# Kernel tuning notes

Measured on AMD Instinct MI355X. Metric: run time of the kernel, lower is better.

## Reference

```python
import jax, jax.numpy as jnp
import numpy as np

# opt hyperparameters (from init_kwargs)
L = 16        # number of multipath taps
M = 64        # number of subcarriers (FFT size for H_t)
N_PILOT = 2   # pilot symbols
V = 100.0     # velocity used for Doppler shift


def setup_inputs() -> dict:
    key = jax.random.key(0)
    k1, k2, k3, k4 = jax.random.split(key, 4)
    N, P, S, MK = 1024, 8, 14, 80
    SMK = S * MK  # 1120
    return {
        "input_real": jax.random.normal(k1, (N, P, SMK), dtype=jnp.float32),
        "input_imag": jax.random.normal(k2, (N, P, SMK), dtype=jnp.float32),
        "cof_real": jax.random.normal(k3, (N, P, L), dtype=jnp.float32),
        "cof_imag": jax.random.normal(k4, (N, P, L), dtype=jnp.float32),
        "Ns": 12,
    }


def reference(input_real, input_imag, cof_real, cof_imag, Ns):
    N, P, SMK = input_real.shape
    S = Ns + N_PILOT
    x = (input_real + 1j * input_imag).astype(jnp.complex64)   # (N,P,SMK)
    cof = (cof_real + 1j * cof_imag).astype(jnp.complex64)      # (N,P,L)

    # H_t: FFT of zero-padded channel taps along delay dim
    cof_zp = jnp.concatenate([cof, jnp.zeros((N, P, M - L), dtype=cof.dtype)], axis=-1)
    H_t = jnp.fft.fft(cof_zp, axis=-1)                          # (N,P,M)

    # Doppler phase shifts: shift[l,s] = exp(i * 2*pi*cos(angle_l)*fd * t_s)
    t = jnp.linspace(0.0, (S - 1) * (0.0005 / 14.0), S)         # (S,)
    carrier_freq = 3.0e9
    max_doppler = V / 3.0e8 * carrier_freq
    angles = jnp.linspace(0.0, 2.0 * np.pi, L)                  # (L,)
    phases = jnp.outer(2.0 * np.pi * jnp.cos(angles) * max_doppler, t)  # (L,S)
    shift = jnp.exp(1j * phases).astype(jnp.complex64)          # (L,S)

    # out[n,p,s,k] = sum_l x[n,p,s,k] * cof[n,p,l] * shift[l,s]
    # The sum over L factors out of the MK dim -> fused weight, avoiding the
    # (N,P,L,S,MK) broadcast intermediate the original materializes.
    weight = jnp.einsum('npl,ls->nps', cof, shift)              # (N,P,S)
    out = x.reshape(N, P, S, -1) * weight[..., None]            # (N,P,S,MK)
    output = out.reshape(N, P, SMK)
    return output, H_t
```

## Files before the change

### kernel.cpp

```cpp
#include <hip/hip_runtime.h>
#include <math.h>

#define L_TAPS 16
#define M_FFT  64
#define SMAX   256
#define SMK_MAX 2048

__global__ __launch_bounds__(256) void channel_kernel(
    const float* __restrict__ xr, const float* __restrict__ xi,
    const float* __restrict__ cr, const float* __restrict__ ci,
    const int*   __restrict__ ns_ptr,
    float* __restrict__ out,
    int NP, int SMK, int interleaved)
{
    __shared__ float  s_cr[L_TAPS], s_ci[L_TAPS];
    __shared__ float2 s_w[SMAX];
    __shared__ unsigned short s_smap[SMK_MAX];

    const int np  = blockIdx.x;
    const int tid = threadIdx.x;
    const int S   = ns_ptr[0] + 2;
    const int MK  = SMK / S;

    if (tid < L_TAPS) {
        s_cr[tid] = cr[(size_t)np * L_TAPS + tid];
        s_ci[tid] = ci[(size_t)np * L_TAPS + tid];
    }
    __syncthreads();

    for (int i = tid; i < SMK; i += 256) {
        s_smap[i] = (unsigned short)(i / MK);
    }

    if (tid < S && tid < SMAX) {
        const float two_pi = 6.2831853071795864f;
        const float dt     = 0.0005f / 14.0f;
        const float fd     = 100.0f / 3.0e8f * 3.0e9f;
        const float t      = tid * dt;
        float wr_ = 0.f, wi_ = 0.f;
        #pragma unroll
        for (int l = 0; l < L_TAPS; ++l) {
            float angle = l * (two_pi / 15.0f);
            float phase = two_pi * __cosf(angle) * fd * t;
            float sp, cp;
            __sincosf(phase, &sp, &cp);
            wr_ += s_cr[l] * cp - s_ci[l] * sp;
            wi_ += s_cr[l] * sp + s_ci[l] * cp;
        }
        s_w[tid] = make_float2(wr_, wi_);
    }

    if (tid >= 64 && tid < 64 + M_FFT) {
        const int m = tid - 64;
        float hr = 0.f, hi = 0.f;
        #pragma unroll
        for (int l = 0; l < L_TAPS; ++l) {
            int ml = (m * l) & (M_FFT - 1);
            float theta = -(float)ml * (6.2831853071795864f / 64.0f);
            float sp, cp;
            __sincosf(theta, &sp, &cp);
            hr += s_cr[l] * cp - s_ci[l] * sp;
            hi += s_cr[l] * sp + s_ci[l] * cp;
        }
        const size_t hbase = (size_t)NP * SMK;
        if (interleaved) {
            ((float2*)out)[hbase + (size_t)np * M_FFT + m] = make_float2(hr, hi);
        } else {
            out[hbase + (size_t)np * M_FFT + m] = hr;
        }
    }
    __syncthreads();

    const size_t base = (size_t)np * SMK;
    if ((MK & 3) == 0 && (SMK & 3) == 0) {
        const float4* xr4 = (const float4*)(xr + base);
        const float4* xi4 = (const float4*)(xi + base);
        const int nvec = SMK >> 2;
        for (int i = tid; i < nvec; i += 256) {
            float4 a = xr4[i];
            float4 b = xi4[i];
            float2 w = s_w[s_smap[i << 2]];
            float4 re;
            re.x = a.x * w.x - b.x * w.y;
            re.y = a.y * w.x - b.y * w.y;
            re.z = a.z * w.x - b.z * w.y;
            re.w = a.w * w.x - b.w * w.y;
            if (interleaved) {
                float2* o = ((float2*)out) + base;
                o[(i << 2) + 0] = make_float2(re.x, a.x * w.y + b.x * w.x);
                o[(i << 2) + 1] = make_float2(re.y, a.y * w.y + b.y * w.x);
                o[(i << 2) + 2] = make_float2(re.z, a.z * w.y + b.z * w.x);
                o[(i << 2) + 3] = make_float2(re.w, a.w * w.y + b.w * w.x);
            } else {
                ((float4*)(out + base))[i] = re;
            }
        }
    } else {
        for (int i = tid; i < SMK; i += 256) {
            float xre = xr[base + i];
            float xim = xi[base + i];
            float2 w  = s_w[s_smap[i]];
            if (interleaved) {
                ((float2*)out)[base + i] = make_float2(xre * w.x - xim * w.y,
                                                       xre * w.y + xim * w.x);
            } else {
                out[base + i] = xre * w.x - xim * w.y;
            }
        }
    }
}

extern "C" void kernel_launch(void* const* d_in, const int* in_sizes, int n_in,
                              void* d_out, int out_size, void* d_ws, size_t ws_size,
                              hipStream_t stream) {
    const float* xr = (const float*)d_in[0];
    const float* xi = (const float*)d_in[1];
    const float* cr = (const float*)d_in[2];
    const float* ci = (const float*)d_in[3];
    const int*   ns = (const int*)  d_in[4];

    const int NP  = in_sizes[2] / L_TAPS;
    const int SMK = in_sizes[0] / NP;

    const int elems = NP * SMK + NP * M_FFT;
    const int interleaved = (out_size == 2 * elems) ? 1 : 0;

    channel_kernel<<<NP, 256, 0, stream>>>(xr, xi, cr, ci, ns,
                                           (float*)d_out, NP, SMK, interleaved);
}
```

Baseline: 23.87 us.

## Split into weight/H_t kernel and grid-stride streaming multiply kernel

The single per-row kernel becomes two kernels. The first computes the per-row Doppler weights into workspace and writes H_t from a shared twiddle table, handling four rows per block. The second is a flat grid-stride elementwise multiply over all rows with float4 loads, so work is no longer tied to one block per row. This removes the per-block smap division table and the redundant sincos work, at the cost of an extra launch and a round trip of the weights through global memory.

```diff
diff --git a/kernel.cpp b/kernel.cpp
--- a/kernel.cpp
+++ b/kernel.cpp
@@ -3,110 +3,110 @@
 
 #define L_TAPS 16
 #define M_FFT  64
-#define SMAX   256
-#define SMK_MAX 2048
 
-__global__ __launch_bounds__(256) void channel_kernel(
-    const float* __restrict__ xr, const float* __restrict__ xi,
+__global__ __launch_bounds__(256) void weight_ht_kernel(
     const float* __restrict__ cr, const float* __restrict__ ci,
     const int*   __restrict__ ns_ptr,
-    float* __restrict__ out,
+    float2* __restrict__ ws,
+    float*  __restrict__ out,
     int NP, int SMK, int interleaved)
 {
-    __shared__ float  s_cr[L_TAPS], s_ci[L_TAPS];
-    __shared__ float2 s_w[SMAX];
-    __shared__ unsigned short s_smap[SMK_MAX];
+    __shared__ float2 s_tw[M_FFT];
+    __shared__ float  s_dop[L_TAPS];
+    __shared__ float2 s_cof[4][L_TAPS];
 
-    const int np  = blockIdx.x;
-    const int tid = threadIdx.x;
-    const int S   = ns_ptr[0] + 2;
-    const int MK  = SMK / S;
+    const int tid  = threadIdx.x;
+    const int S    = ns_ptr[0] + 2;
+    const int row0 = blockIdx.x * 4;
+    const int row  = tid >> 6;
+    const int lane = tid & 63;
+    const int np   = row0 + row;
 
-    if (tid < L_TAPS) {
-        s_cr[tid] = cr[(size_t)np * L_TAPS + tid];
-        s_ci[tid] = ci[(size_t)np * L_TAPS + tid];
+    const float two_pi = 6.2831853071795864f;
+
+    if (tid < 64) {
+        float sp, cp;
+        __sincosf(-(float)tid * (two_pi / 64.0f), &sp, &cp);
+        s_tw[tid] = make_float2(cp, sp);
+    } else if (tid < 64 + L_TAPS) {
+        int l = tid - 64;
+        s_dop[l] = two_pi * __cosf(l * (two_pi / 15.0f)) * (100.0f / 3.0e8f * 3.0e9f);
+    } else if (tid >= 128 && tid < 192) {
+        int r = (tid - 128) >> 4;
+        int l = tid & 15;
+        int npp = row0 + r;
+        if (npp < NP)
+            s_cof[r][l] = make_float2(cr[(size_t)npp * L_TAPS + l],
+                                      ci[(size_t)npp * L_TAPS + l]);
     }
     __syncthreads();
 
-    for (int i = tid; i < SMK; i += 256) {
-        s_smap[i] = (unsigned short)(i / MK);
-    }
+    if (np >= NP) return;
 
-    if (tid < S && tid < SMAX) {
-        const float two_pi = 6.2831853071795864f;
-        const float dt     = 0.0005f / 14.0f;
-        const float fd     = 100.0f / 3.0e8f * 3.0e9f;
-        const float t      = tid * dt;
-        float wr_ = 0.f, wi_ = 0.f;
-        #pragma unroll
-        for (int l = 0; l < L_TAPS; ++l) {
-            float angle = l * (two_pi / 15.0f);
-            float phase = two_pi * __cosf(angle) * fd * t;
-            float sp, cp;
-            __sincosf(phase, &sp, &cp);
-            wr_ += s_cr[l] * cp - s_ci[l] * sp;
-            wi_ += s_cr[l] * sp + s_ci[l] * cp;
-        }
-        s_w[tid] = make_float2(wr_, wi_);
-    }
-
-    if (tid >= 64 && tid < 64 + M_FFT) {
-        const int m = tid - 64;
+    {
+        const int m = lane;
         float hr = 0.f, hi = 0.f;
         #pragma unroll
         for (int l = 0; l < L_TAPS; ++l) {
-            int ml = (m * l) & (M_FFT - 1);
-            float theta = -(float)ml * (6.2831853071795864f / 64.0f);
-            float sp, cp;
-            __sincosf(theta, &sp, &cp);
-            hr += s_cr[l] * cp - s_ci[l] * sp;
-            hi += s_cr[l] * sp + s_ci[l] * cp;
+            float2 c = s_cof[row][l];
+            float2 t = s_tw[(m * l) & (M_FFT - 1)];
+            hr += c.x * t.x - c.y * t.y;
+            hi += c.x * t.y + c.y * t.x;
         }
         const size_t hbase = (size_t)NP * SMK;
-        if (interleaved) {
+        if (interleaved)
             ((float2*)out)[hbase + (size_t)np * M_FFT + m] = make_float2(hr, hi);
-        } else {
+        else
             out[hbase + (size_t)np * M_FFT + m] = hr;
+    }
+
+    if (lane < S) {
+        const float t = lane * (0.0005f / 14.0f);
+        float wr = 0.f, wi = 0.f;
+        #pragma unroll
+        for (int l = 0; l < L_TAPS; ++l) {
+            float sp, cp;
+            __sincosf(s_dop[l] * t, &sp, &cp);
+            float2 c = s_cof[row][l];
+            wr += c.x * cp - c.y * sp;
+            wi += c.x * sp + c.y * cp;
         }
+        ws[np * S + lane] = make_float2(wr, wi);
     }
-    __syncthreads();
+}
 
-    const size_t base = (size_t)np * SMK;
-    if ((MK & 3) == 0 && (SMK & 3) == 0) {
-        const float4* xr4 = (const float4*)(xr + base);
-        const float4* xi4 = (const float4*)(xi + base);
-        const int nvec = SMK >> 2;
-        for (int i = tid; i < nvec; i += 256) {
-            float4 a = xr4[i];
-            float4 b = xi4[i];
-            float2 w = s_w[s_smap[i << 2]];
-            float4 re;
-            re.x = a.x * w.x - b.x * w.y;
-            re.y = a.y * w.x - b.y * w.y;
-            re.z = a.z * w.x - b.z * w.y;
-            re.w = a.w * w.x - b.w * w.y;
-            if (interleaved) {
-                float2* o = ((float2*)out) + base;
-                o[(i << 2) + 0] = make_float2(re.x, a.x * w.y + b.x * w.x);
-                o[(i << 2) + 1] = make_float2(re.y, a.y * w.y + b.y * w.x);
-                o[(i << 2) + 2] = make_float2(re.z, a.z * w.y + b.z * w.x);
-                o[(i << 2) + 3] = make_float2(re.w, a.w * w.y + b.w * w.x);
-            } else {
-                ((float4*)(out + base))[i] = re;
-            }
-        }
-    } else {
-        for (int i = tid; i < SMK; i += 256) {
-            float xre = xr[base + i];
-            float xim = xi[base + i];
-            float2 w  = s_w[s_smap[i]];
-            if (interleaved) {
-                ((float2*)out)[base + i] = make_float2(xre * w.x - xim * w.y,
-                                                       xre * w.y + xim * w.x);
-            } else {
-                out[base + i] = xre * w.x - xim * w.y;
-            }
-        }
+__global__ __launch_bounds__(256) void stream_kernel_v4(
+    const float4* __restrict__ xr4, const float4* __restrict__ xi4,
+    const float2* __restrict__ ws,
+    float4* __restrict__ out4, int nvec, int mkq)
+{
+    const int stride = gridDim.x * blockDim.x;
+    for (int v = blockIdx.x * blockDim.x + threadIdx.x; v < nvec; v += stride) {
+        float4 a = xr4[v];
+        float4 b = xi4[v];
+        float2 w = ws[v / mkq];
+        float4 r;
+        r.x = a.x * w.x - b.x * w.y;
+        r.y = a.y * w.x - b.y * w.y;
+        r.z = a.z * w.x - b.z * w.y;
+        r.w = a.w * w.x - b.w * w.y;
+        out4[v] = r;
+    }
+}
+
+__global__ __launch_bounds__(256) void stream_kernel_scalar(
+    const float* __restrict__ xr, const float* __restrict__ xi,
+    const float2* __restrict__ ws,
+    float* __restrict__ out, int n, int MK, int interleaved)
+{
+    const int stride = gridDim.x * blockDim.x;
+    for (int i = blockIdx.x * blockDim.x + threadIdx.x; i < n; i += stride) {
+        float2 w = ws[i / MK];
+        float  a = xr[i], b = xi[i];
+        if (interleaved)
+            ((float2*)out)[i] = make_float2(a * w.x - b * w.y, a * w.y + b * w.x);
+        else
+            out[i] = a * w.x - b * w.y;
     }
 }
 
@@ -125,6 +125,55 @@
     const int elems = NP * SMK + NP * M_FFT;
     const int interleaved = (out_size == 2 * elems) ? 1 : 0;
 
-    channel_kernel<<<NP, 256, 0, stream>>>(xr, xi, cr, ci, ns,
-                                           (float*)d_out, NP, SMK, interleaved);
+    float2* ws  = (float2*)d_ws;
+    float*  out = (float*)d_out;
+
+    weight_ht_kernel<<<(NP + 3) / 4, 256, 0, stream>>>(cr, ci, ns, ws, out,
+                                                       NP, SMK, interleaved);
+
+    (void)ws_size;
+    extern __global__ void stream_dispatch(const float4*, const float4*,
+                                           const float2*, const int*,
+                                           float*, int, int, int);
+    stream_dispatch<<<2048, 256, 0, stream>>>((const float4*)xr, (const float4*)xi,
+                                              ws, ns, out, NP, SMK, interleaved);
 }
+
+__global__ __launch_bounds__(256) void stream_dispatch(
+    const float4* __restrict__ xr4, const float4* __restrict__ xi4,
+    const float2* __restrict__ ws, const int* __restrict__ ns_ptr,
+    float* __restrict__ out, int NP, int SMK, int interleaved)
+{
+    const int S  = ns_ptr[0] + 2;
+    const int MK = SMK / S;
+    const int n  = NP * SMK;
+    const int stride = gridDim.x * blockDim.x;
+
+    if (!interleaved && (MK & 3) == 0) {
+        const int nvec = n >> 2;
+        const int mkq  = MK >> 2;
+        float4* out4 = (float4*)out;
+        for (int v = blockIdx.x * blockDim.x + threadIdx.x; v < nvec; v += stride) {
+            float4 a = xr4[v];
+            float4 b = xi4[v];
+            float2 w = ws[v / mkq];
+            float4 r;
+            r.x = a.x * w.x - b.x * w.y;
+            r.y = a.y * w.x - b.y * w.y;
+            r.z = a.z * w.x - b.z * w.y;
+            r.w = a.w * w.x - b.w * w.y;
+            out4[v] = r;
+        }
+    } else {
+        const float* xr = (const float*)xr4;
+        const float* xi = (const float*)xi4;
+        for (int i = blockIdx.x * blockDim.x + threadIdx.x; i < n; i += stride) {
+            float2 w = ws[i / MK];
+            float  a = xr[i], b = xi[i];
+            if (interleaved)
+                ((float2*)out)[i] = make_float2(a * w.x - b * w.y, a * w.y + b * w.x);
+            else
+                out[i] = a * w.x - b * w.y;
+        }
+    }
+}
```

Result: slower. 28.87 us (+21.0%).

## Process four rows per block with shared twiddles and shuffle-reduced Doppler weights

Applied to the files above, without the earlier changes.

Each block now handles four (n,p) rows instead of one, so there are a quarter as many blocks and the setup work is amortised over more streaming work. Twiddle factors and Doppler rates are precomputed once in shared memory, and the per-symbol weights are computed in parallel across taps with a 16-lane shuffle reduction. The symbol index map is replaced by an integer divide, and the interleaved complex output path is dropped, so the kernel always writes the real part only. This relies on the output format never needing interleaving, and fewer blocks may reduce how many CUs are kept busy.

```diff
diff --git a/kernel.cpp b/kernel.cpp
--- a/kernel.cpp
+++ b/kernel.cpp
@@ -3,109 +3,122 @@
 
 #define L_TAPS 16
 #define M_FFT  64
-#define SMAX   256
-#define SMK_MAX 2048
+#define ROWS   4
+#define SMAX   128
 
-__global__ __launch_bounds__(256) void channel_kernel(
+__global__ __launch_bounds__(256) void channel_fused(
     const float* __restrict__ xr, const float* __restrict__ xi,
     const float* __restrict__ cr, const float* __restrict__ ci,
     const int*   __restrict__ ns_ptr,
     float* __restrict__ out,
-    int NP, int SMK, int interleaved)
+    int NP, int SMK)
 {
-    __shared__ float  s_cr[L_TAPS], s_ci[L_TAPS];
-    __shared__ float2 s_w[SMAX];
-    __shared__ unsigned short s_smap[SMK_MAX];
+    __shared__ float2 s_tw[M_FFT];
+    __shared__ float  s_dop[L_TAPS];
+    __shared__ float2 s_cof[ROWS][L_TAPS];
+    __shared__ float2 s_w[ROWS * SMAX];
 
-    const int np  = blockIdx.x;
-    const int tid = threadIdx.x;
-    const int S   = ns_ptr[0] + 2;
-    const int MK  = SMK / S;
+    const int tid  = threadIdx.x;
+    const int S    = ns_ptr[0] + 2;
+    const int MK   = SMK / S;
+    const int row0 = blockIdx.x * ROWS;
 
-    if (tid < L_TAPS) {
-        s_cr[tid] = cr[(size_t)np * L_TAPS + tid];
-        s_ci[tid] = ci[(size_t)np * L_TAPS + tid];
+    const float two_pi = 6.2831853071795864f;
+
+    if (tid < M_FFT) {
+        float sp, cp;
+        __sincosf(-(float)tid * (two_pi / (float)M_FFT), &sp, &cp);
+        s_tw[tid] = make_float2(cp, sp);
+    } else if (tid < M_FFT + L_TAPS) {
+        int l = tid - M_FFT;
+        s_dop[l] = two_pi * __cosf((float)l * (two_pi / (float)(L_TAPS - 1)))
+                 * (100.0f / 3.0e8f * 3.0e9f);
+    } else if (tid >= 128 && tid < 128 + ROWS * L_TAPS) {
+        int r = (tid - 128) >> 4, l = tid & 15;
+        int npp = row0 + r;
+        if (npp < NP)
+            s_cof[r][l] = make_float2(cr[(size_t)npp * L_TAPS + l],
+                                      ci[(size_t)npp * L_TAPS + l]);
     }
     __syncthreads();
 
-    for (int i = tid; i < SMK; i += 256) {
-        s_smap[i] = (unsigned short)(i / MK);
+    if (S <= SMAX) {
+        const int l = tid & 15;
+        for (int s = tid >> 4; s < S; s += 16) {
+            float sp, cp;
+            __sincosf(s_dop[l] * ((float)s * (0.0005f / 14.0f)), &sp, &cp);
+            #pragma unroll
+            for (int r = 0; r < ROWS; ++r) {
+                float2 c = s_cof[r][l];
+                float pr = c.x * cp - c.y * sp;
+                float pi_ = c.x * sp + c.y * cp;
+                #pragma unroll
+                for (int off = 8; off; off >>= 1) {
+                    pr  += __shfl_xor(pr,  off, 16);
+                    pi_ += __shfl_xor(pi_, off, 16);
+                }
+                if (l == 0 && row0 + r < NP) s_w[r * S + s] = make_float2(pr, pi_);
+            }
+        }
     }
 
-    if (tid < S && tid < SMAX) {
-        const float two_pi = 6.2831853071795864f;
-        const float dt     = 0.0005f / 14.0f;
-        const float fd     = 100.0f / 3.0e8f * 3.0e9f;
-        const float t      = tid * dt;
-        float wr_ = 0.f, wi_ = 0.f;
-        #pragma unroll
-        for (int l = 0; l < L_TAPS; ++l) {
-            float angle = l * (two_pi / 15.0f);
-            float phase = two_pi * __cosf(angle) * fd * t;
-            float sp, cp;
-            __sincosf(phase, &sp, &cp);
-            wr_ += s_cr[l] * cp - s_ci[l] * sp;
-            wi_ += s_cr[l] * sp + s_ci[l] * cp;
-        }
-        s_w[tid] = make_float2(wr_, wi_);
-    }
-
-    if (tid >= 64 && tid < 64 + M_FFT) {
-        const int m = tid - 64;
-        float hr = 0.f, hi = 0.f;
-        #pragma unroll
-        for (int l = 0; l < L_TAPS; ++l) {
-            int ml = (m * l) & (M_FFT - 1);
-            float theta = -(float)ml * (6.2831853071795864f / 64.0f);
-            float sp, cp;
-            __sincosf(theta, &sp, &cp);
-            hr += s_cr[l] * cp - s_ci[l] * sp;
-            hi += s_cr[l] * sp + s_ci[l] * cp;
-        }
-        const size_t hbase = (size_t)NP * SMK;
-        if (interleaved) {
-            ((float2*)out)[hbase + (size_t)np * M_FFT + m] = make_float2(hr, hi);
-        } else {
-            out[hbase + (size_t)np * M_FFT + m] = hr;
+    {
+        const int r = tid >> 6, m = tid & 63;
+        const int npp = row0 + r;
+        if (npp < NP) {
+            float hr = 0.f;
+            #pragma unroll
+            for (int l = 0; l < L_TAPS; ++l) {
+                float2 c = s_cof[r][l];
+                float2 t = s_tw[(m * l) & (M_FFT - 1)];
+                hr += c.x * t.x - c.y * t.y;
+            }
+            out[(size_t)NP * SMK + (size_t)npp * M_FFT + m] = hr;
         }
     }
     __syncthreads();
 
-    const size_t base = (size_t)np * SMK;
-    if ((MK & 3) == 0 && (SMK & 3) == 0) {
-        const float4* xr4 = (const float4*)(xr + base);
-        const float4* xi4 = (const float4*)(xi + base);
-        const int nvec = SMK >> 2;
-        for (int i = tid; i < nvec; i += 256) {
-            float4 a = xr4[i];
-            float4 b = xi4[i];
-            float2 w = s_w[s_smap[i << 2]];
-            float4 re;
-            re.x = a.x * w.x - b.x * w.y;
-            re.y = a.y * w.x - b.y * w.y;
-            re.z = a.z * w.x - b.z * w.y;
-            re.w = a.w * w.x - b.w * w.y;
-            if (interleaved) {
-                float2* o = ((float2*)out) + base;
-                o[(i << 2) + 0] = make_float2(re.x, a.x * w.y + b.x * w.x);
-                o[(i << 2) + 1] = make_float2(re.y, a.y * w.y + b.y * w.x);
-                o[(i << 2) + 2] = make_float2(re.z, a.z * w.y + b.z * w.x);
-                o[(i << 2) + 3] = make_float2(re.w, a.w * w.y + b.w * w.x);
-            } else {
-                ((float4*)(out + base))[i] = re;
-            }
+    const int rows_here = min(ROWS, NP - row0);
+    if (S <= SMAX && (MK & 3) == 0 && (SMK & 3) == 0) {
+        const int   mkq   = MK >> 2;
+        const int   limit = (rows_here * SMK) >> 2;
+        const size_t gb   = (size_t)row0 * (SMK >> 2);
+        const float4* xr4 = (const float4*)xr + gb;
+        const float4* xi4 = (const float4*)xi + gb;
+        float4*       o4  = (float4*)out + gb;
+        for (int v = tid; v < limit; v += 256) {
+            float4 a = xr4[v];
+            float4 b = xi4[v];
+            float2 w = s_w[(unsigned)v / (unsigned)mkq];
+            float4 r4;
+            r4.x = a.x * w.x - b.x * w.y;
+            r4.y = a.y * w.x - b.y * w.y;
+            r4.z = a.z * w.x - b.z * w.y;
+            r4.w = a.w * w.x - b.w * w.y;
+            o4[v] = r4;
+        }
+    } else if (S <= SMAX) {
+        const size_t gb = (size_t)row0 * SMK;
+        const int limit = rows_here * SMK;
+        for (int i = tid; i < limit; i += 256) {
+            float2 w = s_w[(unsigned)i / (unsigned)MK];
+            out[gb + i] = xr[gb + i] * w.x - xi[gb + i] * w.y;
         }
     } else {
-        for (int i = tid; i < SMK; i += 256) {
-            float xre = xr[base + i];
-            float xim = xi[base + i];
-            float2 w  = s_w[s_smap[i]];
-            if (interleaved) {
-                ((float2*)out)[base + i] = make_float2(xre * w.x - xim * w.y,
-                                                       xre * w.y + xim * w.x);
-            } else {
-                out[base + i] = xre * w.x - xim * w.y;
+        const size_t gb = (size_t)row0 * SMK;
+        const int limit = rows_here * SMK;
+        for (int i = tid; i < limit; i += 256) {
+            int r = i / SMK, s = (i - r * SMK) / MK;
+            float wr = 0.f, wi = 0.f;
+            #pragma unroll
+            for (int l = 0; l < L_TAPS; ++l) {
+                float sp, cp;
+                __sincosf(s_dop[l] * ((float)s * (0.0005f / 14.0f)), &sp, &cp);
+                float2 c = s_cof[r][l];
+                wr += c.x * cp - c.y * sp;
+                wi += c.x * sp + c.y * cp;
             }
+            out[gb + i] = xr[gb + i] * wr - xi[gb + i] * wi;
         }
     }
 }
@@ -121,10 +134,8 @@
 
     const int NP  = in_sizes[2] / L_TAPS;
     const int SMK = in_sizes[0] / NP;
+    (void)d_ws; (void)ws_size; (void)out_size; (void)n_in;
 
-    const int elems = NP * SMK + NP * M_FFT;
-    const int interleaved = (out_size == 2 * elems) ? 1 : 0;
-
-    channel_kernel<<<NP, 256, 0, stream>>>(xr, xi, cr, ci, ns,
-                                           (float*)d_out, NP, SMK, interleaved);
+    channel_fused<<<(NP + ROWS - 1) / ROWS, 256, 0, stream>>>(
+        xr, xi, cr, ci, ns, (float*)d_out, NP, SMK);
 }
```

Result: slower. 25.59 us (+7.2%).
